# Kernel optimization log

Hardware: AMD Instinct MI355X
Metric: run time of the kernel (lower is better)

The kernel has to match this reference:

```python
import jax, jax.numpy as jnp
import numpy as np

B = 128
DIM = 1024


def setup_inputs() -> dict:
    key = jax.random.key(0)
    k1, k2 = jax.random.split(key)
    return {
        "input1": jax.random.normal(k1, (B, DIM), dtype=jnp.float32),
        "input2": jax.random.normal(k2, (B, DIM), dtype=jnp.float32),
    }


def reference(input1, input2):
    # Original torch module computes, via a dim x dim x dim permutation tensor:
    #   cc[b, i] = sum_t input1[b, (i - t) % dim] * input2[b, t]   (circular convolution)
    # then sums over the batch and reshapes to [1, 1, dim].
    dim = input1.shape[1]
    # idx[i, t] = (i - t) mod dim  -> circulant gather of input1
    idx = (jnp.arange(dim)[:, None] - jnp.arange(dim)[None, :]) % dim
    gathered = input1[:, idx]                      # [B, dim, dim]
    cc = jnp.einsum('bit,bt->bi', gathered, input2)  # per-batch circular conv [B, dim]
    sum_rep = jnp.sum(cc, axis=0)                  # [dim]
    return sum_rep[None, None, :]                  # [1, 1, dim]
```

## Files before the change

### kernel.cpp

```cpp
#include <hip/hip_runtime.h>


#define CC_D 1024

__global__ __launch_bounds__(256) void cc_partial_kernel(
    const float* __restrict__ X, const float* __restrict__ Y,
    float* __restrict__ ws) {
  const int blk    = blockIdx.x;
  const int b      = blk >> 3;
  const int tslice = blk & 7;
  const int tid    = threadIdx.x;
  const int ig     = tid & 127;
  const int ts     = tid >> 7;

  __shared__ __align__(16) float xsh[2 * CC_D];

  const float4 xv = ((const float4*)(X + b * CC_D))[tid];
  ((float4*)xsh)[tid]       = xv;
  ((float4*)xsh)[tid + 256] = xv;
  __syncthreads();

  const int ts_u   = __builtin_amdgcn_readfirstlane(ts);
  const int tstart = tslice * 128 + ts_u * 64;
  const float* yb  = Y + b * CC_D + tstart;

  const float* base0 = xsh + CC_D + 8 * ig - tstart - 8;

  float acc[8];
#pragma unroll
  for (int q = 0; q < 8; ++q) acc[q] = 0.f;

  float W[16];
#pragma unroll
  for (int j = 0; j < 4; ++j) {
    const float4 w = ((const float4*)base0)[j];
    W[4 * j + 0] = w.x; W[4 * j + 1] = w.y;
    W[4 * j + 2] = w.z; W[4 * j + 3] = w.w;
  }

#pragma unroll
  for (int g = 0; g < 8; ++g) {
    float y[8];
#pragma unroll
    for (int j = 0; j < 2; ++j) {
      const float4 yv = ((const float4*)(yb + 8 * g))[j];
      y[4 * j + 0] = yv.x; y[4 * j + 1] = yv.y;
      y[4 * j + 2] = yv.z; y[4 * j + 3] = yv.w;
    }

#pragma unroll
    for (int r = 0; r < 8; ++r)
#pragma unroll
      for (int q = 0; q < 8; ++q)
        acc[q] += W[8 + q - r] * y[r];

    if (g < 7) {
#pragma unroll
      for (int j = 0; j < 8; ++j) W[8 + j] = W[j];
      const float* nb = base0 - 8 * (g + 1);
      const float4 w0 = ((const float4*)nb)[0];
      const float4 w1 = ((const float4*)nb)[1];
      W[0] = w0.x; W[1] = w0.y; W[2] = w0.z; W[3] = w0.w;
      W[4] = w1.x; W[5] = w1.y; W[6] = w1.z; W[7] = w1.w;
    }
  }

  __syncthreads();
  float4* st = (float4*)(xsh + ts * CC_D + 8 * ig);
  st[0] = make_float4(acc[0], acc[1], acc[2], acc[3]);
  st[1] = make_float4(acc[4], acc[5], acc[6], acc[7]);
  __syncthreads();

  const float4 s0 = ((const float4*)xsh)[tid];
  const float4 s1 = ((const float4*)(xsh + CC_D))[tid];
  float4 r;
  r.x = s0.x + s1.x; r.y = s0.y + s1.y;
  r.z = s0.z + s1.z; r.w = s0.w + s1.w;
  ((float4*)(ws + (size_t)blk * CC_D))[tid] = r;
}

__global__ __launch_bounds__(256) void cc_reduce_kernel(
    const float* __restrict__ ws, float* __restrict__ out) {
  const int j   = blockIdx.x;
  const int tid = threadIdx.x;

  __shared__ float4 red[256];

  float4 s = make_float4(0.f, 0.f, 0.f, 0.f);
#pragma unroll
  for (int p = 0; p < 4; ++p) {
    const float4 v =
        *(const float4*)(ws + (size_t)(tid + 256 * p) * CC_D + 4 * j);
    s.x += v.x; s.y += v.y; s.z += v.z; s.w += v.w;
  }
  red[tid] = s;
  __syncthreads();

  for (int st = 128; st > 0; st >>= 1) {
    if (tid < st) {
      const float4 o = red[tid + st];
      red[tid].x += o.x; red[tid].y += o.y;
      red[tid].z += o.z; red[tid].w += o.w;
    }
    __syncthreads();
  }

  if (tid == 0) ((float4*)out)[j] = red[0];
}

extern "C" void kernel_launch(void* const* d_in, const int* in_sizes, int n_in,
                              void* d_out, int out_size, void* d_ws,
                              size_t ws_size, hipStream_t stream) {
  const float* X = (const float*)d_in[0];
  const float* Y = (const float*)d_in[1];
  float* out = (float*)d_out;
  float* ws  = (float*)d_ws;

  cc_partial_kernel<<<1024, 256, 0, stream>>>(X, Y, ws);
  cc_reduce_kernel<<<256, 256, 0, stream>>>(ws, out);
}
```

Before: 73.11 us.

## Use 512-thread blocks with swizzled LDS X copy and Y staged in shared memory

Doubles the threads per block so each wave covers 32 t-values instead of 64, which halves the per-thread inner loop and adds a four-way shared-memory reduction at the end. The doubled X row in LDS is now stored with an XOR-like float4 swizzle to avoid bank conflicts on the strided circulant reads. Y values are staged once in LDS instead of being read from global memory by every thread. The costs are more partial sums to reduce inside each block and higher LDS use per block.

```diff
diff --git a/kernel.cpp b/kernel.cpp
--- a/kernel.cpp
+++ b/kernel.cpp
@@ -3,7 +3,11 @@
 
 #define CC_D 1024
 
-__global__ __launch_bounds__(256) void cc_partial_kernel(
+__device__ __forceinline__ int swz(int f) {
+  return (f & ~7) | ((f + (f >> 3)) & 7);
+}
+
+__global__ __launch_bounds__(512, 8) void cc_partial_kernel(
     const float* __restrict__ X, const float* __restrict__ Y,
     float* __restrict__ ws) {
   const int blk    = blockIdx.x;
@@ -13,40 +17,43 @@
   const int ig     = tid & 127;
   const int ts     = tid >> 7;
 
-  __shared__ __align__(16) float xsh[2 * CC_D];
+  __shared__ __align__(16) float smem[4096 + 128];
+  float4* sm4 = (float4*)smem;
+  float*  ysh = smem + 4096;
 
-  const float4 xv = ((const float4*)(X + b * CC_D))[tid];
-  ((float4*)xsh)[tid]       = xv;
-  ((float4*)xsh)[tid + 256] = xv;
+  if (tid < 256) {
+    const float4 v = ((const float4*)(X + b * CC_D))[tid];
+    sm4[swz(tid)]       = v;
+    sm4[swz(tid + 256)] = v;
+  }
+  if (tid < 32) {
+    ((float4*)ysh)[tid] =
+        ((const float4*)(Y + b * CC_D + tslice * 128))[tid];
+  }
   __syncthreads();
 
-  const int ts_u   = __builtin_amdgcn_readfirstlane(ts);
-  const int tstart = tslice * 128 + ts_u * 64;
-  const float* yb  = Y + b * CC_D + tstart;
+  const int ts_u = __builtin_amdgcn_readfirstlane(ts);
+  const int t0   = tslice * 128 + ts_u * 32;
 
-  const float* base0 = xsh + CC_D + 8 * ig - tstart - 8;
+  const int f0 = 254 + 2 * ig - (t0 >> 2);
+
+  float W[16];
+#pragma unroll
+  for (int m = 0; m < 4; ++m) {
+    const float4 w = sm4[swz(f0 + m)];
+    W[4 * m + 0] = w.x; W[4 * m + 1] = w.y;
+    W[4 * m + 2] = w.z; W[4 * m + 3] = w.w;
+  }
 
   float acc[8];
 #pragma unroll
   for (int q = 0; q < 8; ++q) acc[q] = 0.f;
 
-  float W[16];
 #pragma unroll
-  for (int j = 0; j < 4; ++j) {
-    const float4 w = ((const float4*)base0)[j];
-    W[4 * j + 0] = w.x; W[4 * j + 1] = w.y;
-    W[4 * j + 2] = w.z; W[4 * j + 3] = w.w;
-  }
-
-#pragma unroll
-  for (int g = 0; g < 8; ++g) {
-    float y[8];
-#pragma unroll
-    for (int j = 0; j < 2; ++j) {
-      const float4 yv = ((const float4*)(yb + 8 * g))[j];
-      y[4 * j + 0] = yv.x; y[4 * j + 1] = yv.y;
-      y[4 * j + 2] = yv.z; y[4 * j + 3] = yv.w;
-    }
+  for (int g = 0; g < 4; ++g) {
+    const float4 ya = ((const float4*)ysh)[ts_u * 8 + 2 * g];
+    const float4 yb = ((const float4*)ysh)[ts_u * 8 + 2 * g + 1];
+    const float y[8] = {ya.x, ya.y, ya.z, ya.w, yb.x, yb.y, yb.z, yb.w};
 
 #pragma unroll
     for (int r = 0; r < 8; ++r)
@@ -54,29 +61,31 @@
       for (int q = 0; q < 8; ++q)
         acc[q] += W[8 + q - r] * y[r];
 
-    if (g < 7) {
+    if (g < 3) {
 #pragma unroll
       for (int j = 0; j < 8; ++j) W[8 + j] = W[j];
-      const float* nb = base0 - 8 * (g + 1);
-      const float4 w0 = ((const float4*)nb)[0];
-      const float4 w1 = ((const float4*)nb)[1];
+      const float4 w0 = sm4[swz(f0 - 2 * (g + 1))];
+      const float4 w1 = sm4[swz(f0 - 2 * (g + 1) + 1)];
       W[0] = w0.x; W[1] = w0.y; W[2] = w0.z; W[3] = w0.w;
       W[4] = w1.x; W[5] = w1.y; W[6] = w1.z; W[7] = w1.w;
     }
   }
 
   __syncthreads();
-  float4* st = (float4*)(xsh + ts * CC_D + 8 * ig);
+  float4* st = (float4*)(smem + ts * CC_D + 8 * ig);
   st[0] = make_float4(acc[0], acc[1], acc[2], acc[3]);
   st[1] = make_float4(acc[4], acc[5], acc[6], acc[7]);
   __syncthreads();
 
-  const float4 s0 = ((const float4*)xsh)[tid];
-  const float4 s1 = ((const float4*)(xsh + CC_D))[tid];
-  float4 r;
-  r.x = s0.x + s1.x; r.y = s0.y + s1.y;
-  r.z = s0.z + s1.z; r.w = s0.w + s1.w;
-  ((float4*)(ws + (size_t)blk * CC_D))[tid] = r;
+  if (tid < 256) {
+    float4 s = make_float4(0.f, 0.f, 0.f, 0.f);
+#pragma unroll
+    for (int sidx = 0; sidx < 4; ++sidx) {
+      const float4 v = sm4[sidx * 256 + tid];
+      s.x += v.x; s.y += v.y; s.z += v.z; s.w += v.w;
+    }
+    ((float4*)ws)[blk * 256 + tid] = s;
+  }
 }
 
 __global__ __launch_bounds__(256) void cc_reduce_kernel(
@@ -89,8 +98,7 @@
   float4 s = make_float4(0.f, 0.f, 0.f, 0.f);
 #pragma unroll
   for (int p = 0; p < 4; ++p) {
-    const float4 v =
-        *(const float4*)(ws + (size_t)(tid + 256 * p) * CC_D + 4 * j);
+    const float4 v = ((const float4*)ws)[(size_t)(tid + 256 * p) * 256 + j];
     s.x += v.x; s.y += v.y; s.z += v.z; s.w += v.w;
   }
   red[tid] = s;
@@ -116,6 +124,6 @@
   float* out = (float*)d_out;
   float* ws  = (float*)d_ws;
 
-  cc_partial_kernel<<<1024, 256, 0, stream>>>(X, Y, ws);
+  cc_partial_kernel<<<1024, 512, 0, stream>>>(X, Y, ws);
   cc_reduce_kernel<<<256, 256, 0, stream>>>(ws, out);
 }
```

New measurement: 70.35 us. -3.8%, faster.
